# Performance work log

Hardware: AMD Instinct MI355X
Metric: run time of the kernel (lower is better)

Reference implementation:

```python
import jax, jax.numpy as jnp
import numpy as np

EPS = 1e-5
B, C, H, W = 64, 256, 64, 64


def _masked_mean(p9, r0, r1, c0, c1):
    # p9: [B,3,3,9,H,W]; r0,r1: [B,3] int row bounds (per i); c0,c1: [B,3] int col bounds (per j)
    Hh, Ww = p9.shape[-2], p9.shape[-1]
    rows = jnp.arange(Hh, dtype=jnp.int32)
    cols = jnp.arange(Ww, dtype=jnp.int32)
    mr = (rows[None, None, :] >= r0[..., None]) & (rows[None, None, :] < r1[..., None])  # [B,3,H]
    mc = (cols[None, None, :] >= c0[..., None]) & (cols[None, None, :] < c1[..., None])  # [B,3,W]
    mask = (mr[:, :, None, :, None] & mc[:, None, :, None, :]).astype(p9.dtype)  # [B,3,3,H,W]
    cnt = mask.sum((-2, -1))  # [B,3,3]
    s = jnp.einsum('bijkhw,bijhw->bijk', p9, mask)
    return jnp.where(cnt[..., None] > 0, s / jnp.maximum(cnt, 1.0)[..., None], 0.0)  # [B,3,3,9]


def _subj_obj_bounds(bbox, Hh, Ww):
    # bbox: [B,4] = [y0,y1,x0,x1] normalized
    y0, y1, x0, x1 = bbox[:, 0], bbox[:, 1], bbox[:, 2], bbox[:, 3]
    ch = (y1 - y0) / 3.0
    cw = (x1 - x0) / 3.0
    idx = jnp.arange(3, dtype=bbox.dtype)
    r0 = jnp.floor(Hh * (y0[:, None] + idx * ch[:, None])).astype(jnp.int32)
    r1 = jnp.floor(Hh * (y0[:, None] + (idx + 1.0) * ch[:, None])).astype(jnp.int32)
    dr = r1 <= r0
    r1n = jnp.where(dr & (r1 < Hh - 1), r1 + 1, r1)
    r0n = jnp.where(dr & (r1 >= Hh - 1), r0 - 1, r0)
    c0 = jnp.floor(Ww * (x0[:, None] + idx * cw[:, None])).astype(jnp.int32)
    c1 = jnp.floor(Ww * (x0[:, None] + (idx + 1.0) * cw[:, None])).astype(jnp.int32)
    dc = c1 <= c0
    c1n = jnp.where(dc & (c1 < Ww), c1 + 1, c1)
    c0n = jnp.where(dc & (c1 >= Ww), c0 - 1, c0)
    return r0n, r1n, c0n, c1n


def _joint_bounds(bbox, bbox_s, bbox_o, Hh, Ww):
    # intersection of bbox with the 3x3 cells of union(bbox_s, bbox_o)
    uy0 = jnp.minimum(bbox_s[:, 0], bbox_o[:, 0])
    uy1 = jnp.maximum(bbox_s[:, 1], bbox_o[:, 1])
    ux0 = jnp.minimum(bbox_s[:, 2], bbox_o[:, 2])
    ux1 = jnp.maximum(bbox_s[:, 3], bbox_o[:, 3])
    ch = (uy1 - uy0) / 3.0
    cw = (ux1 - ux0) / 3.0
    idx = jnp.arange(3, dtype=bbox.dtype)
    ylo = uy0[:, None] + idx * ch[:, None]
    yhi = uy0[:, None] + (idx + 1.0) * ch[:, None]
    xlo = ux0[:, None] + idx * cw[:, None]
    xhi = ux0[:, None] + (idx + 1.0) * cw[:, None]
    r0 = jnp.floor(Hh * jnp.maximum(bbox[:, 0][:, None], ylo)).astype(jnp.int32)
    r1 = jnp.floor(Hh * jnp.minimum(bbox[:, 1][:, None], yhi)).astype(jnp.int32)
    c0 = jnp.floor(Ww * jnp.maximum(bbox[:, 2][:, None], xlo)).astype(jnp.int32)
    c1 = jnp.floor(Ww * jnp.minimum(bbox[:, 3][:, None], xhi)).astype(jnp.int32)
    return r0, r1, c0, c1


def setup_inputs() -> dict:
    key = jax.random.key(0)
    ks = jax.random.split(key, 16)
    feat = jax.random.normal(ks[0], (B, C, H, W), dtype=jnp.float32)

    def make_bbox(k):
        k1, k2, k3, k4 = jax.random.split(k, 4)
        y0 = jax.random.uniform(k1, (B,), minval=0.0, maxval=0.4)
        y1 = jnp.minimum(y0 + jax.random.uniform(k2, (B,), minval=0.3, maxval=0.55), 0.99)
        x0 = jax.random.uniform(k3, (B,), minval=0.0, maxval=0.4)
        x1 = jnp.minimum(x0 + jax.random.uniform(k4, (B,), minval=0.3, maxval=0.55), 0.99)
        return jnp.stack([y0, y1, x0, x1], axis=1).astype(jnp.float32)

    bbox_s = make_bbox(ks[1])
    bbox_o = make_bbox(ks[2])
    predicate = jax.random.uniform(ks[3], (B, 9), dtype=jnp.float32)
    conv_w = jax.random.normal(ks[4], (324, 256), dtype=jnp.float32) * 0.02
    conv_b = jax.random.normal(ks[5], (324,), dtype=jnp.float32) * 0.02
    bn2_g = jax.random.uniform(ks[6], (324,), minval=0.5, maxval=1.5)
    bn2_b = jax.random.normal(ks[7], (324,)) * 0.02
    bn2_m = jax.random.normal(ks[8], (324,)) * 0.02
    bn2_v = jax.random.uniform(ks[9], (324,), minval=0.5, maxval=1.5)
    fc1_w = jax.random.normal(ks[10], (40, 81), dtype=jnp.float32) * 0.1
    fc1_b = jnp.zeros((40,), jnp.float32)
    bn1_g = jax.random.uniform(ks[11], (40,), minval=0.5, maxval=1.5)
    bn1_b = jax.random.normal(ks[12], (40,)) * 0.02
    bn1_m = jax.random.normal(ks[13], (40,)) * 0.02
    bn1_v = jax.random.uniform(ks[14], (40,), minval=0.5, maxval=1.5)
    fc2_w = jax.random.normal(ks[15], (9, 40), dtype=jnp.float32) * 0.1
    fc2_b = jnp.zeros((9,), jnp.float32)
    return dict(feat=feat, bbox_s=bbox_s, bbox_o=bbox_o, predicate=predicate,
                conv_w=conv_w, conv_b=conv_b, bn2_g=bn2_g, bn2_b=bn2_b, bn2_m=bn2_m, bn2_v=bn2_v,
                fc1_w=fc1_w, fc1_b=fc1_b, bn1_g=bn1_g, bn1_b=bn1_b, bn1_m=bn1_m, bn1_v=bn1_v,
                fc2_w=fc2_w, fc2_b=fc2_b)


def reference(feat, bbox_s, bbox_o, predicate, conv_w, conv_b, bn2_g, bn2_b, bn2_m, bn2_v,
              fc1_w, fc1_b, bn1_g, bn1_b, bn1_m, bn1_v, fc2_w, fc2_b):
    # 1x1 conv 256 -> 324, then BatchNorm2d (inference mode)
    prs = jnp.einsum('bchw,oc->bohw', feat, conv_w) + conv_b[None, :, None, None]
    prs = (prs - bn2_m[None, :, None, None]) * (bn2_g / jnp.sqrt(bn2_v + EPS))[None, :, None, None] + bn2_b[None, :, None, None]
    Bb, _, Hh, Ww = prs.shape
    # channel layout: start = i*27 + j*9 + k  ->  reshape to [B,3,3,9,H,W]
    def bank(lo):
        return prs[:, lo:lo + 81].reshape(Bb, 3, 3, 9, Hh, Ww)
    prs_s, prs_o, prs_js, prs_jo = bank(0), bank(81), bank(162), bank(243)

    feature_s = _masked_mean(prs_s, *_subj_obj_bounds(bbox_s, Hh, Ww))
    feature_o = _masked_mean(prs_o, *_subj_obj_bounds(bbox_o, Hh, Ww))
    feature_j = (_masked_mean(prs_js, *_joint_bounds(bbox_s, bbox_s, bbox_o, Hh, Ww)) +
                 _masked_mean(prs_jo, *_joint_bounds(bbox_o, bbox_s, bbox_o, Hh, Ww)))

    f = feature_s + feature_o + feature_j            # [B,3,3,9]
    f = jnp.transpose(f, (0, 3, 1, 2)).reshape(Bb, 81)  # torch layout [B,9,3,3] flattened

    h = f @ fc1_w.T + fc1_b
    h = (h - bn1_m) * (bn1_g / jnp.sqrt(bn1_v + EPS)) + bn1_b
    logits = h @ fc2_w.T + fc2_b
    return jnp.sum(logits * predicate, axis=1)
```

## Files before the change

### kernel.cpp

```cpp
#include <hip/hip_runtime.h>
#include <hip/hip_bf16.h>
#include <cstdint>

#define BB 64
#define CC 256
#define EPSF 1e-5f
#define PLANES 4
#define ZROW 24
#define SSTR 65

__device__ __forceinline__ void region_bounds(int bank, int i, int j,
                                              float sy0, float sy1, float sx0, float sx1,
                                              float oy0, float oy1, float ox0, float ox1,
                                              int& r0, int& r1, int& c0, int& c1) {
    float fi = (float)i, fj = (float)j;
    if (bank < 2) {
        float y0 = bank ? oy0 : sy0, y1 = bank ? oy1 : sy1;
        float x0 = bank ? ox0 : sx0, x1 = bank ? ox1 : sx1;
        float ch = __fdiv_rn(__fsub_rn(y1, y0), 3.0f);
        float cw = __fdiv_rn(__fsub_rn(x1, x0), 3.0f);
        int R0 = (int)floorf(__fmul_rn(64.0f, __fadd_rn(y0, __fmul_rn(fi, ch))));
        int R1 = (int)floorf(__fmul_rn(64.0f, __fadd_rn(y0, __fmul_rn(__fadd_rn(fi, 1.0f), ch))));
        bool dr = (R1 <= R0);
        r1 = (dr && (R1 < 63)) ? R1 + 1 : R1;
        r0 = (dr && (R1 >= 63)) ? R0 - 1 : R0;
        int C0 = (int)floorf(__fmul_rn(64.0f, __fadd_rn(x0, __fmul_rn(fj, cw))));
        int C1 = (int)floorf(__fmul_rn(64.0f, __fadd_rn(x0, __fmul_rn(__fadd_rn(fj, 1.0f), cw))));
        bool dc = (C1 <= C0);
        c1 = (dc && (C1 < 64)) ? C1 + 1 : C1;
        c0 = (dc && (C1 >= 64)) ? C0 - 1 : C0;
    } else {
        float by0 = (bank == 2) ? sy0 : oy0, by1 = (bank == 2) ? sy1 : oy1;
        float bx0 = (bank == 2) ? sx0 : ox0, bx1 = (bank == 2) ? sx1 : ox1;
        float uy0 = fminf(sy0, oy0), uy1 = fmaxf(sy1, oy1);
        float ux0 = fminf(sx0, ox0), ux1 = fmaxf(sx1, ox1);
        float ch = __fdiv_rn(__fsub_rn(uy1, uy0), 3.0f);
        float cw = __fdiv_rn(__fsub_rn(ux1, ux0), 3.0f);
        float ylo = __fadd_rn(uy0, __fmul_rn(fi, ch));
        float yhi = __fadd_rn(uy0, __fmul_rn(__fadd_rn(fi, 1.0f), ch));
        float xlo = __fadd_rn(ux0, __fmul_rn(fj, cw));
        float xhi = __fadd_rn(ux0, __fmul_rn(__fadd_rn(fj, 1.0f), cw));
        r0 = (int)floorf(__fmul_rn(64.0f, fmaxf(by0, ylo)));
        r1 = (int)floorf(__fmul_rn(64.0f, fminf(by1, yhi)));
        c0 = (int)floorf(__fmul_rn(64.0f, fmaxf(bx0, xlo)));
        c1 = (int)floorf(__fmul_rn(64.0f, fminf(bx1, xhi)));
    }
}

__global__ __launch_bounds__(64, 4) void k_region_sums(const float* __restrict__ feat,
                                                       const float* __restrict__ bbox_s,
                                                       const float* __restrict__ bbox_o,
                                                       float* __restrict__ M) {
    int l = threadIdx.x;
    int pid0 = blockIdx.x * PLANES;
    int b = pid0 >> 8;

    float sy0 = bbox_s[b * 4 + 0], sy1 = bbox_s[b * 4 + 1];
    float sx0 = bbox_s[b * 4 + 2], sx1 = bbox_s[b * 4 + 3];
    float oy0 = bbox_o[b * 4 + 0], oy1 = bbox_o[b * 4 + 1];
    float ox0 = bbox_o[b * 4 + 2], ox1 = bbox_o[b * 4 + 3];

    int myb = l / 9, myrest = l % 9, myi = myrest / 3, myj = myrest % 3;

    unsigned long long rowmask = 0ull;
    int my_r0c = 0, my_r1c = 0;
    #pragma unroll
    for (int bk = 0; bk < 4; ++bk) {
        #pragma unroll
        for (int i = 0; i < 3; ++i) {
            int r0, r1, c0, c1;
            region_bounds(bk, i, 0, sy0, sy1, sx0, sx1, oy0, oy1, ox0, ox1, r0, r1, c0, c1);
            int r0c = max(r0, 0), r1c = min(r1, 64);
            if (r1c >= 1) rowmask |= 1ull << (r1c - 1);
            if (r0c >= 1) rowmask |= 1ull << (r0c - 1);
            if (bk == myb && i == myi) { my_r0c = r0c; my_r1c = r1c; }
        }
    }
    unsigned int mlo = __builtin_amdgcn_readfirstlane((unsigned int)rowmask);
    unsigned int mhi = __builtin_amdgcn_readfirstlane((unsigned int)(rowmask >> 32));
    unsigned long long smask = (((unsigned long long)mhi) << 32) | mlo;

    int cl = 0, ch = 0, idx0 = ZROW, idx1 = ZROW;
    if (l < 36) {
        int r0, r1, c0, c1;
        region_bounds(myb, myi, myj, sy0, sy1, sx0, sx1, oy0, oy1, ox0, ox1, r0, r1, c0, c1);
        cl = max(c0, 0); ch = min(c1, 64);
        if (my_r1c <= my_r0c) {
            ch = cl;
        } else {
            idx1 = __popcll(smask & ((1ull << (my_r1c - 1)) - 1ull));
            idx0 = (my_r0c > 0) ? (int)__popcll(smask & ((1ull << (my_r0c - 1)) - 1ull)) : ZROW;
        }
    }

    __shared__ float S[(ZROW + 1) * SSTR];
    S[ZROW * SSTR + l] = 0.0f;
    __syncthreads();

    const float* pf = feat + (size_t)pid0 * 4096 + l;
    for (int p = 0; p < PLANES; ++p) {
        float x[32];
        float run = 0.0f;
        int slot = 0;
        #pragma unroll
        for (int h = 0; h < 32; ++h) x[h] = pf[h * 64];
        #pragma unroll
        for (int h = 0; h < 32; ++h) {
            run += x[h];
            if ((smask >> h) & 1ull) { S[slot * SSTR + l] = run; ++slot; }
        }
        #pragma unroll
        for (int h = 0; h < 32; ++h) x[h] = pf[(32 + h) * 64];
        #pragma unroll
        for (int h = 0; h < 32; ++h) {
            run += x[h];
            if ((smask >> (32 + h)) & 1ull) { S[slot * SSTR + l] = run; ++slot; }
        }
        __syncthreads();

        if (l < 36) {
            float s = 0.0f;
            for (int w = cl; w < ch; ++w)
                s += S[idx1 * SSTR + w] - S[idx0 * SSTR + w];
            M[(size_t)(pid0 + p) * 36 + l] = s;
        }
        __syncthreads();
        pf += 4096;
    }
}

__global__ __launch_bounds__(384) void k_head(const float* __restrict__ M,
                                              const float* __restrict__ bbox_s,
                                              const float* __restrict__ bbox_o,
                                              const float* __restrict__ conv_w,
                                              const float* __restrict__ conv_b,
                                              const float* __restrict__ g2,
                                              const float* __restrict__ b2,
                                              const float* __restrict__ m2,
                                              const float* __restrict__ v2,
                                              const float* __restrict__ fc1_w,
                                              const float* __restrict__ fc1_b,
                                              const float* __restrict__ g1,
                                              const float* __restrict__ b1,
                                              const float* __restrict__ m1,
                                              const float* __restrict__ v1,
                                              const float* __restrict__ fc2_w,
                                              const float* __restrict__ fc2_b,
                                              const float* __restrict__ pred,
                                              float* __restrict__ out) {
    int b = blockIdx.x;
    int t = threadIdx.x;

    __shared__ float MlT[36 * 264];
    __shared__ float val[324];
    __shared__ float fv[81];
    __shared__ float hv[40];
    __shared__ float lg[9];

    for (int i = t; i < 36 * 256; i += 384) {
        int r = i >> 8, c = i & 255;
        MlT[r * 264 + c] = M[(size_t)b * (256 * 36) + c * 36 + r];
    }
    __syncthreads();

    if (t < 324) {
        int region = t / 9, k = t - region * 9;
        int bank = region / 9, ij = region - bank * 9;
        int ii = ij / 3, jj = ij % 3;
        int o = bank * 81 + ii * 27 + jj * 9 + k;

        float sy0 = bbox_s[b * 4 + 0], sy1 = bbox_s[b * 4 + 1];
        float sx0 = bbox_s[b * 4 + 2], sx1 = bbox_s[b * 4 + 3];
        float oy0 = bbox_o[b * 4 + 0], oy1 = bbox_o[b * 4 + 1];
        float ox0 = bbox_o[b * 4 + 2], ox1 = bbox_o[b * 4 + 3];
        int r0, r1, c0, c1;
        region_bounds(bank, ii, jj, sy0, sy1, sx0, sx1, oy0, oy1, ox0, ox1, r0, r1, c0, c1);
        int nrows = max(0, min(r1, 64) - max(r0, 0));
        int ncols = max(0, min(c1, 64) - max(c0, 0));
        float cnt = (float)(nrows * ncols);

        float v = 0.0f;
        if (cnt > 0.0f) {
            const float4* wv = (const float4*)(conv_w + o * 256);
            const float4* mv = (const float4*)(&MlT[region * 264]);
            float4 a4 = make_float4(0.f, 0.f, 0.f, 0.f);
            #pragma unroll 8
            for (int c4 = 0; c4 < 64; ++c4) {
                float4 wq = wv[c4], mq = mv[c4];
                a4.x += wq.x * mq.x; a4.y += wq.y * mq.y;
                a4.z += wq.z * mq.z; a4.w += wq.w * mq.w;
            }
            float dot = (a4.x + a4.y) + (a4.z + a4.w);
            float mean = dot / cnt;
            float sc = g2[o] / sqrtf(v2[o] + EPSF);
            v = (mean + conv_b[o] - m2[o]) * sc + b2[o];
        }
        val[region * 9 + k] = v;
    }
    __syncthreads();

    if (t < 81) {
        int k = t / 9, ij = t - k * 9;
        fv[t] = val[(0 + ij) * 9 + k] + val[(9 + ij) * 9 + k] +
                val[(18 + ij) * 9 + k] + val[(27 + ij) * 9 + k];
    }
    __syncthreads();

    if (t < 40) {
        float h = fc1_b[t];
        for (int u = 0; u < 81; ++u) h += fv[u] * fc1_w[t * 81 + u];
        h = (h - m1[t]) * (g1[t] / sqrtf(v1[t] + EPSF)) + b1[t];
        hv[t] = h;
    }
    __syncthreads();

    if (t < 9) {
        float lgt = fc2_b[t];
        for (int u = 0; u < 40; ++u) lgt += hv[u] * fc2_w[t * 40 + u];
        lg[t] = lgt * pred[b * 9 + t];
    }
    __syncthreads();

    if (t == 0) {
        float s = 0.0f;
        for (int i = 0; i < 9; ++i) s += lg[i];
        out[b] = s;
    }
}

extern "C" void kernel_launch(void* const* d_in, const int* in_sizes, int n_in,
                              void* d_out, int out_size, void* d_ws, size_t ws_size,
                              hipStream_t stream) {
    const float* feat   = (const float*)d_in[0];
    const float* bbox_s = (const float*)d_in[1];
    const float* bbox_o = (const float*)d_in[2];
    const float* pred   = (const float*)d_in[3];
    const float* conv_w = (const float*)d_in[4];
    const float* conv_b = (const float*)d_in[5];
    const float* g2     = (const float*)d_in[6];
    const float* b2     = (const float*)d_in[7];
    const float* m2     = (const float*)d_in[8];
    const float* v2     = (const float*)d_in[9];
    const float* fc1_w  = (const float*)d_in[10];
    const float* fc1_b  = (const float*)d_in[11];
    const float* g1     = (const float*)d_in[12];
    const float* b1     = (const float*)d_in[13];
    const float* m1     = (const float*)d_in[14];
    const float* v1     = (const float*)d_in[15];
    const float* fc2_w  = (const float*)d_in[16];
    const float* fc2_b  = (const float*)d_in[17];
    float* out = (float*)d_out;

    float* M = (float*)d_ws;

    k_region_sums<<<(BB * CC) / PLANES, 64, 0, stream>>>(feat, bbox_s, bbox_o, M);
    k_head<<<BB, 384, 0, stream>>>(M, bbox_s, bbox_o, conv_w, conv_b, g2, b2, m2, v2,
                                   fc1_w, fc1_b, g1, b1, m1, v1, fc2_w, fc2_b,
                                   pred, out);
}
```

Baseline: 63.02 us.

## Skip loading rows and columns outside any region, split head into dot and MLP kernels

The region-sum kernel now builds a wave-uniform mask of rows covered by any region and a per-lane flag for columns covered by any region. It loads feature values only for those rows and lanes, which cuts global memory traffic when the boxes are small. M is re-laid out region-major so the head can be split into a 256-block dot-product kernel (one block per batch and bank) plus a small MLP kernel. This adds an extra launch and an intermediate buffer in exchange for more parallelism in the head.

```diff
diff --git a/kernel.cpp b/kernel.cpp
--- a/kernel.cpp
+++ b/kernel.cpp
@@ -8,6 +8,7 @@
 #define PLANES 4
 #define ZROW 24
 #define SSTR 65
+#define NPLANES (BB * CC)
 
 __device__ __forceinline__ void region_bounds(int bank, int i, int j,
                                               float sy0, float sy1, float sx0, float sx1,
@@ -60,36 +61,50 @@
     float oy0 = bbox_o[b * 4 + 0], oy1 = bbox_o[b * 4 + 1];
     float ox0 = bbox_o[b * 4 + 2], ox1 = bbox_o[b * 4 + 3];
 
-    int myb = l / 9, myrest = l % 9, myi = myrest / 3, myj = myrest % 3;
-
-    unsigned long long rowmask = 0ull;
-    int my_r0c = 0, my_r1c = 0;
+    int myb = l / 9, rest = l % 9, myi = rest / 3, myj = rest % 3;
+
+    unsigned long long needm = 0ull, snapm = 0ull;
+    int my_r0c = 0, my_r1c = 0, mycl = 0, mych = 0;
+    bool colact = false;
     #pragma unroll
     for (int bk = 0; bk < 4; ++bk) {
         #pragma unroll
-        for (int i = 0; i < 3; ++i) {
+        for (int idx = 0; idx < 3; ++idx) {
             int r0, r1, c0, c1;
-            region_bounds(bk, i, 0, sy0, sy1, sx0, sx1, oy0, oy1, ox0, ox1, r0, r1, c0, c1);
+            region_bounds(bk, idx, idx, sy0, sy1, sx0, sx1, oy0, oy1, ox0, ox1,
+                          r0, r1, c0, c1);
             int r0c = max(r0, 0), r1c = min(r1, 64);
-            if (r1c >= 1) rowmask |= 1ull << (r1c - 1);
-            if (r0c >= 1) rowmask |= 1ull << (r0c - 1);
-            if (bk == myb && i == myi) { my_r0c = r0c; my_r1c = r1c; }
-        }
-    }
-    unsigned int mlo = __builtin_amdgcn_readfirstlane((unsigned int)rowmask);
-    unsigned int mhi = __builtin_amdgcn_readfirstlane((unsigned int)(rowmask >> 32));
-    unsigned long long smask = (((unsigned long long)mhi) << 32) | mlo;
-
-    int cl = 0, ch = 0, idx0 = ZROW, idx1 = ZROW;
+            if (r1c > r0c) {
+                unsigned long long hi = (r1c >= 64) ? ~0ull : ((1ull << r1c) - 1ull);
+                unsigned long long lo = (1ull << r0c) - 1ull;
+                needm |= hi ^ lo;
+                snapm |= 1ull << (r1c - 1);
+                if (r0c >= 1) snapm |= 1ull << (r0c - 1);
+            }
+            int clc = max(c0, 0), chc = min(c1, 64);
+            if (chc > clc) colact = colact || (l >= clc && l < chc);
+            if (bk == myb && idx == myi) { my_r0c = r0c; my_r1c = r1c; }
+            if (bk == myb && idx == myj) { mycl = max(c0, 0); mych = min(c1, 64); }
+        }
+    }
+    {
+        unsigned int a = __builtin_amdgcn_readfirstlane((unsigned int)needm);
+        unsigned int bm = __builtin_amdgcn_readfirstlane((unsigned int)(needm >> 32));
+        needm = (((unsigned long long)bm) << 32) | a;
+        unsigned int c = __builtin_amdgcn_readfirstlane((unsigned int)snapm);
+        unsigned int d = __builtin_amdgcn_readfirstlane((unsigned int)(snapm >> 32));
+        snapm = (((unsigned long long)d) << 32) | c;
+    }
+
+    int cl = 0, chx = 0, idx0 = ZROW, idx1 = ZROW;
     if (l < 36) {
-        int r0, r1, c0, c1;
-        region_bounds(myb, myi, myj, sy0, sy1, sx0, sx1, oy0, oy1, ox0, ox1, r0, r1, c0, c1);
-        cl = max(c0, 0); ch = min(c1, 64);
+        cl = mycl; chx = mych;
         if (my_r1c <= my_r0c) {
-            ch = cl;
+            chx = cl;
         } else {
-            idx1 = __popcll(smask & ((1ull << (my_r1c - 1)) - 1ull));
-            idx0 = (my_r0c > 0) ? (int)__popcll(smask & ((1ull << (my_r0c - 1)) - 1ull)) : ZROW;
+            idx1 = (int)__popcll(snapm & ((1ull << (my_r1c - 1)) - 1ull));
+            idx0 = (my_r0c > 0) ? (int)__popcll(snapm & ((1ull << (my_r0c - 1)) - 1ull))
+                                : ZROW;
         }
     }
 
@@ -102,70 +117,65 @@
         float x[32];
         float run = 0.0f;
         int slot = 0;
-        #pragma unroll
-        for (int h = 0; h < 32; ++h) x[h] = pf[h * 64];
-        #pragma unroll
-        for (int h = 0; h < 32; ++h) {
-            run += x[h];
-            if ((smask >> h) & 1ull) { S[slot * SSTR + l] = run; ++slot; }
-        }
-        #pragma unroll
-        for (int h = 0; h < 32; ++h) x[h] = pf[(32 + h) * 64];
-        #pragma unroll
-        for (int h = 0; h < 32; ++h) {
-            run += x[h];
-            if ((smask >> (32 + h)) & 1ull) { S[slot * SSTR + l] = run; ++slot; }
+
+        #pragma unroll
+        for (int h = 0; h < 32; ++h) {
+            float v = 0.0f;
+            if (((needm >> h) & 1ull) && colact) v = pf[h * 64];
+            x[h] = v;
+        }
+        #pragma unroll
+        for (int h = 0; h < 32; ++h) {
+            if ((needm >> h) & 1ull) run += x[h];
+            if ((snapm >> h) & 1ull) { S[slot * SSTR + l] = run; ++slot; }
+        }
+        #pragma unroll
+        for (int h = 0; h < 32; ++h) {
+            float v = 0.0f;
+            if (((needm >> (h + 32)) & 1ull) && colact) v = pf[(h + 32) * 64];
+            x[h] = v;
+        }
+        #pragma unroll
+        for (int h = 0; h < 32; ++h) {
+            if ((needm >> (h + 32)) & 1ull) run += x[h];
+            if ((snapm >> (h + 32)) & 1ull) { S[slot * SSTR + l] = run; ++slot; }
         }
         __syncthreads();
 
         if (l < 36) {
             float s = 0.0f;
-            for (int w = cl; w < ch; ++w)
+            for (int w = cl; w < chx; ++w)
                 s += S[idx1 * SSTR + w] - S[idx0 * SSTR + w];
-            M[(size_t)(pid0 + p) * 36 + l] = s;
+            M[(size_t)l * NPLANES + pid0 + p] = s;
         }
         __syncthreads();
         pf += 4096;
     }
 }
 
-__global__ __launch_bounds__(384) void k_head(const float* __restrict__ M,
-                                              const float* __restrict__ bbox_s,
-                                              const float* __restrict__ bbox_o,
-                                              const float* __restrict__ conv_w,
-                                              const float* __restrict__ conv_b,
-                                              const float* __restrict__ g2,
-                                              const float* __restrict__ b2,
-                                              const float* __restrict__ m2,
-                                              const float* __restrict__ v2,
-                                              const float* __restrict__ fc1_w,
-                                              const float* __restrict__ fc1_b,
-                                              const float* __restrict__ g1,
-                                              const float* __restrict__ b1,
-                                              const float* __restrict__ m1,
-                                              const float* __restrict__ v1,
-                                              const float* __restrict__ fc2_w,
-                                              const float* __restrict__ fc2_b,
-                                              const float* __restrict__ pred,
-                                              float* __restrict__ out) {
-    int b = blockIdx.x;
+__global__ __launch_bounds__(128) void k_head_dot(const float* __restrict__ M,
+                                                  const float* __restrict__ bbox_s,
+                                                  const float* __restrict__ bbox_o,
+                                                  const float* __restrict__ conv_w,
+                                                  const float* __restrict__ conv_b,
+                                                  const float* __restrict__ g2,
+                                                  const float* __restrict__ b2,
+                                                  const float* __restrict__ m2,
+                                                  const float* __restrict__ v2,
+                                                  float* __restrict__ val) {
+    int blk = blockIdx.x;
+    int b = blk >> 2, bank = blk & 3;
     int t = threadIdx.x;
 
-    __shared__ float MlT[36 * 264];
-    __shared__ float val[324];
-    __shared__ float fv[81];
-    __shared__ float hv[40];
-    __shared__ float lg[9];
-
-    for (int i = t; i < 36 * 256; i += 384) {
-        int r = i >> 8, c = i & 255;
-        MlT[r * 264 + c] = M[(size_t)b * (256 * 36) + c * 36 + r];
-    }
-    __syncthreads();
-
-    if (t < 324) {
-        int region = t / 9, k = t - region * 9;
-        int bank = region / 9, ij = region - bank * 9;
+    __shared__ float MlT9[9 * 264];
+    for (int i = t; i < 9 * 256; i += 128) {
+        int ij = i >> 8, c = i & 255;
+        MlT9[ij * 264 + c] = M[(size_t)(bank * 9 + ij) * NPLANES + (b << 8) + c];
+    }
+    __syncthreads();
+
+    if (t < 81) {
+        int ij = t / 9, k = t - ij * 9;
         int ii = ij / 3, jj = ij % 3;
         int o = bank * 81 + ii * 27 + jj * 9 + k;
 
@@ -174,7 +184,8 @@
         float oy0 = bbox_o[b * 4 + 0], oy1 = bbox_o[b * 4 + 1];
         float ox0 = bbox_o[b * 4 + 2], ox1 = bbox_o[b * 4 + 3];
         int r0, r1, c0, c1;
-        region_bounds(bank, ii, jj, sy0, sy1, sx0, sx1, oy0, oy1, ox0, ox1, r0, r1, c0, c1);
+        region_bounds(bank, ii, jj, sy0, sy1, sx0, sx1, oy0, oy1, ox0, ox1,
+                      r0, r1, c0, c1);
         int nrows = max(0, min(r1, 64) - max(r0, 0));
         int ncols = max(0, min(c1, 64) - max(c0, 0));
         float cnt = (float)(nrows * ncols);
@@ -182,7 +193,7 @@
         float v = 0.0f;
         if (cnt > 0.0f) {
             const float4* wv = (const float4*)(conv_w + o * 256);
-            const float4* mv = (const float4*)(&MlT[region * 264]);
+            const float4* mv = (const float4*)(&MlT9[ij * 264]);
             float4 a4 = make_float4(0.f, 0.f, 0.f, 0.f);
             #pragma unroll 8
             for (int c4 = 0; c4 < 64; ++c4) {
@@ -195,14 +206,33 @@
             float sc = g2[o] / sqrtf(v2[o] + EPSF);
             v = (mean + conv_b[o] - m2[o]) * sc + b2[o];
         }
-        val[region * 9 + k] = v;
-    }
-    __syncthreads();
+        val[b * 324 + bank * 81 + t] = v;
+    }
+}
+
+__global__ __launch_bounds__(128) void k_head_mlp(const float* __restrict__ val,
+                                                  const float* __restrict__ fc1_w,
+                                                  const float* __restrict__ fc1_b,
+                                                  const float* __restrict__ g1,
+                                                  const float* __restrict__ b1,
+                                                  const float* __restrict__ m1,
+                                                  const float* __restrict__ v1,
+                                                  const float* __restrict__ fc2_w,
+                                                  const float* __restrict__ fc2_b,
+                                                  const float* __restrict__ pred,
+                                                  float* __restrict__ out) {
+    int b = blockIdx.x;
+    int t = threadIdx.x;
+
+    __shared__ float fv[81];
+    __shared__ float hv[40];
+    __shared__ float lg[9];
 
     if (t < 81) {
         int k = t / 9, ij = t - k * 9;
-        fv[t] = val[(0 + ij) * 9 + k] + val[(9 + ij) * 9 + k] +
-                val[(18 + ij) * 9 + k] + val[(27 + ij) * 9 + k];
+        const float* vb = val + b * 324;
+        fv[t] = vb[0 * 81 + ij * 9 + k] + vb[1 * 81 + ij * 9 + k] +
+                vb[2 * 81 + ij * 9 + k] + vb[3 * 81 + ij * 9 + k];
     }
     __syncthreads();
 
@@ -251,10 +281,13 @@
     const float* fc2_b  = (const float*)d_in[17];
     float* out = (float*)d_out;
 
-    float* M = (float*)d_ws;
+    char* ws = (char*)d_ws;
+    float* M   = (float*)ws;
+    float* val = (float*)(ws + 2359296);
 
     k_region_sums<<<(BB * CC) / PLANES, 64, 0, stream>>>(feat, bbox_s, bbox_o, M);
-    k_head<<<BB, 384, 0, stream>>>(M, bbox_s, bbox_o, conv_w, conv_b, g2, b2, m2, v2,
-                                   fc1_w, fc1_b, g1, b1, m1, v1, fc2_w, fc2_b,
-                                   pred, out);
-}
+    k_head_dot<<<BB * 4, 128, 0, stream>>>(M, bbox_s, bbox_o, conv_w, conv_b,
+                                           g2, b2, m2, v2, val);
+    k_head_mlp<<<BB, 128, 0, stream>>>(val, fc1_w, fc1_b, g1, b1, m1, v1,
+                                       fc2_w, fc2_b, pred, out);
+}
```

After: 54.75 us. 13.1% less time.
